# Optimization experiments

Measured on AMD Instinct MI355X. Metric: run time of the kernel, lower is better.

## Reference

```python
import jax, jax.numpy as jnp
import numpy as np

BATCH = 8192
NUM_FEATURES = 2048
NUM_CLASSES = 10
NUM_LAYERS = 2
LOGIT_SCALE = 5.0
INV_SQRT2 = 1.0 / np.sqrt(2.0)


def setup_inputs() -> dict:
    key = jax.random.key(0)
    k1, k2 = jax.random.split(key)
    # input feature phases in [-pi, pi), one oscillator thread per feature
    x = jax.random.uniform(k1, (BATCH, NUM_FEATURES), jnp.float32, -np.pi, np.pi)
    # trainable phase shifts: (num_stacks * num_layers * num_features,) ~ U(-pi, pi)
    weights = jax.random.uniform(k2, (NUM_LAYERS * NUM_FEATURES,), jnp.float32, -np.pi, np.pi)
    return {"x": x, "weights": weights}


def _vpc_forward(x, weights):
    # x: (B, N) phases; state z_i = e^{i x_i} with unit amplitude
    B, N = x.shape
    w = weights.reshape(NUM_LAYERS, N)  # per-layer shift parameters
    z = jnp.exp(1j * x)  # complex64 state vector, shape (B, N)
    for layer in range(NUM_LAYERS):
        # shift: rotate every thread phase by its trainable weight
        z = z * jnp.exp(1j * w[layer])  # broadcast (N,) over batch
        # mix: Hadamard-like 2x2 unitary on adjacent pairs (0,1),(2,3),...
        a = z[:, 0::2]
        b = z[:, 1::2]
        z = jnp.stack(((a + b) * INV_SQRT2, (a - b) * INV_SQRT2), axis=-1).reshape(B, N)
        # dft: global unitary DFT across the N threads
        z = jnp.fft.fft(z, norm="ortho")
    phases = jnp.arctan2(jnp.imag(z), jnp.real(z))  # (B, N)
    # multi-class readout: sin-smoothed phases of first K threads -> softmax
    logits = jnp.sin(phases[:, :NUM_CLASSES]) * LOGIT_SCALE
    return jax.nn.softmax(logits, axis=-1)  # (B, K)


def reference(x, weights):
    return _vpc_forward(x, weights)
```

## Files before the change

kernel.cpp:

```cpp
#include <hip/hip_runtime.h>
#include <math.h>

#define NF       2048
#define NC       10
#define THREADS  256

typedef float f2 __attribute__((ext_vector_type(2)));
typedef float f4 __attribute__((ext_vector_type(4)));

__device__ __forceinline__ f2 mk2(float a, float b){ f2 r; r.x=a; r.y=b; return r; }

__device__ __forceinline__ int swz(int i) { return i ^ (((i >> 4) & 7) << 1); }

__device__ __forceinline__ f2 cmul(f2 a, f2 b){
    f2 t = mk2(a.x, a.x) * b;
    return mk2(a.y, a.y) * mk2(-b.y, b.x) + t;
}
__device__ __forceinline__ f2 mul_mi(f2 d){ return mk2(d.y, -d.x); }
__device__ __forceinline__ f2 mul_w1(f2 d){
    const float C = 0.70710678118654752f;
    return (d + mk2(d.y, -d.x)) * mk2(C, C);
}
__device__ __forceinline__ f2 mul_w3(f2 d){
    const float C = 0.70710678118654752f;
    return (mk2(d.y, -d.y) - mk2(d.x, d.x)) * mk2(C, C);
}

template<int S>
__device__ __forceinline__ void stage8_ip(f2* __restrict__ buf,
                                          const f2* __restrict__ twl,
                                          int tid, int rbase)
{
    __syncthreads();
    f2 a0 = buf[rbase       ];
    f2 a1 = buf[rbase +  256];
    f2 a2 = buf[rbase +  512];
    f2 a3 = buf[rbase +  768];
    f2 a4 = buf[rbase + 1024];
    f2 a5 = buf[rbase + 1280];
    f2 a6 = buf[rbase + 1536];
    f2 a7 = buf[rbase + 1792];
    const int q  = tid & (S - 1);
    const int pb = tid ^ q;
    f2 w1 = twl[pb];
    __syncthreads();
    f2 u0 = a0+a4, u1 = a0-a4;
    f2 u2 = a1+a5, u3 = mul_w1(a1-a5);
    f2 u4 = a2+a6, u5 = mul_mi(a2-a6);
    f2 u6 = a3+a7, u7 = mul_w3(a3-a7);
    f2 v0 = u0+u4, v2 = u0-u4;
    f2 v1 = u1+u5, v3 = u1-u5;
    f2 v4 = u2+u6, v6 = mul_mi(u2-u6);
    f2 v5 = u3+u7, v7 = mul_mi(u3-u7);
    const int base = q + 8 * pb;
    buf[swz(base)] = v0+v4;
    f2 y4 = v0-v4;
    f2 w2 = cmul(w1,w1);
    f2 w4 = cmul(w2,w2);
    buf[swz(base + 4*S)] = cmul(y4,w4);
    f2 y1 = v1+v5, y5 = v1-v5;
    buf[swz(base +   S)] = cmul(y1,w1);
    f2 w5 = cmul(w4,w1);
    buf[swz(base + 5*S)] = cmul(y5,w5);
    f2 y2 = v2+v6, y6 = v2-v6;
    buf[swz(base + 2*S)] = cmul(y2,w2);
    f2 w6 = cmul(w4,w2);
    buf[swz(base + 6*S)] = cmul(y6,w6);
    f2 y3 = v3+v7, y7 = v3-v7;
    f2 w3 = cmul(w2,w1);
    buf[swz(base + 3*S)] = cmul(y3,w3);
    f2 w7 = cmul(w4,w3);
    buf[swz(base + 7*S)] = cmul(y7,w7);
}

__device__ __forceinline__ void stage8_trunc(f2* __restrict__ buf,
                                             const f2* __restrict__ twl,
                                             int tid, int rbase)
{
    __syncthreads();
    f2 a0 = buf[rbase       ];
    f2 a1 = buf[rbase +  256];
    f2 a2 = buf[rbase +  512];
    f2 a3 = buf[rbase +  768];
    f2 a4 = buf[rbase + 1024];
    f2 a5 = buf[rbase + 1280];
    f2 a6 = buf[rbase + 1536];
    f2 a7 = buf[rbase + 1792];
    const int q  = tid & 7;
    const int pb = tid ^ q;
    f2 w1 = twl[pb];
    __syncthreads();
    const int base = q + 8 * pb;
    buf[swz(base)] = ((a0+a4) + (a2+a6)) + ((a1+a5) + (a3+a7));
    if (q < 2) {
        f2 u1 = a0-a4;
        f2 u3 = mul_w1(a1-a5);
        f2 u5 = mul_mi(a2-a6);
        f2 u7 = mul_w3(a3-a7);
        buf[swz(base + 8)] = cmul((u1+u5) + (u3+u7), w1);
    }
}

__device__ __forceinline__ void stage4_rot_ip(f2* __restrict__ buf,
                                              const f2* __restrict__ w1r,
                                              int tid, int r2base)
{
    __syncthreads();
    f4 R0 = *(const f4*)&buf[r2base       ];
    f4 R1 = *(const f4*)&buf[r2base +  512];
    f4 R2 = *(const f4*)&buf[r2base + 1024];
    f4 R3 = *(const f4*)&buf[r2base + 1536];
    f2 u0 = R0.lo, v0 = R0.hi;
    f2 u1 = R1.lo, v1 = R1.hi;
    f2 u2 = R2.lo, v2 = R2.hi;
    f2 u3 = R3.lo, v3 = R3.hi;
    f2 us0 = u0+u2, us1 = u1+u3;
    f2 ud0 = u0-u2, ud1 = mul_mi(u1-u3);
    f2 vs0 = v0+v2, vs1 = v1+v3;
    f2 vd0 = v0-v2, vd1 = mul_mi(v1-v3);
    f2 uy[4] = { us0+us1, ud0+ud1, us0-us1, ud0-ud1 };
    f2 vy[4] = { vs0+vs1, vd0+vd1, vs0-vs1, vd0-vd1 };
    #pragma unroll
    for (int k = 0; k < 4; ++k) {
        f2 wv = w1r[tid + 256*k];
        float s0, c0, s1, c1;
        __sincosf(wv.x, &s0, &c0);
        __sincosf(wv.y, &s1, &c1);
        f2 z0 = cmul(uy[k], mk2(c0,s0));
        f2 z1 = cmul(vy[k], mk2(c1,s1));
        f4 o; o.lo = z0+z1; o.hi = z0-z1;
        *(f4*)&buf[r2base + 512*k] = o;
    }
}

__global__ __launch_bounds__(THREADS, 8) void vpc_kernel(
        const float* __restrict__ x, const float* __restrict__ w,
        float* __restrict__ out) {
    __shared__ __align__(16) f2 A[NF];
    __shared__ __align__(16) f2 twl[256];
    __shared__ float smax[NC];
    const int tid    = threadIdx.x;
    const int row    = blockIdx.x;
    const int rbase  = swz(tid);
    const int r2base = swz(2*tid);

    {
        float a = -(float)tid * (float)(M_PI / 1024.0);
        float s, c;
        __sincosf(a, &s, &c);
        twl[tid] = mk2(c, s);
    }

    const f4* xr4 = (const f4*)(x + (size_t)row * NF);
    const f4* wr4 = (const f4*)w;
    #pragma unroll
    for (int i = 0; i < 2; ++i) {
        const int g = tid + 256*i;
        f4 xv = xr4[g];
        f4 wv = wr4[g];
        float s0,c0,s1,c1,s2,c2,s3,c3;
        __sincosf(xv.x + wv.x, &s0, &c0);
        __sincosf(xv.y + wv.y, &s1, &c1);
        __sincosf(xv.z + wv.z, &s2, &c2);
        __sincosf(xv.w + wv.w, &s3, &c3);
        f2 z0 = mk2(c0,s0), z1 = mk2(c1,s1);
        f2 z2 = mk2(c2,s2), z3 = mk2(c3,s3);
        f4 o0; o0.lo = z0+z1; o0.hi = z0-z1;
        f4 o1; o1.lo = z2+z3; o1.hi = z2-z3;
        *(f4*)&A[swz(4*g)]     = o0;
        *(f4*)&A[swz(4*g + 2)] = o1;
    }

    stage8_ip<1> (A, twl, tid, rbase);
    stage8_ip<8> (A, twl, tid, rbase);
    stage8_ip<64>(A, twl, tid, rbase);
    stage4_rot_ip(A, (const f2*)(w + NF), tid, r2base);

    stage8_ip<1>(A, twl, tid, rbase);
    stage8_trunc(A, twl, tid, rbase);

    __syncthreads();
    if (tid < NC) {
        f2 acc = mk2(0.f, 0.f);
        #pragma unroll 8
        for (int r = 0; r < 32; ++r) {
            int addr = (tid + 64*r) ^ ((r & 1) << 3);
            acc = acc + A[addr];
        }
        float mag = sqrtf(acc.x*acc.x + acc.y*acc.y);
        smax[tid] = 5.0f * acc.y / fmaxf(mag, 1e-30f);
    }
    __syncthreads();
    if (tid < NC) {
        float l = smax[tid];
        float mx = smax[0];
        #pragma unroll
        for (int j = 1; j < NC; ++j) mx = fmaxf(mx, smax[j]);
        float s = 0.f;
        #pragma unroll
        for (int j = 0; j < NC; ++j) s += __expf(smax[j] - mx);
        out[(size_t)row * NC + tid] = __expf(l - mx) / s;
    }
}

extern "C" void kernel_launch(void* const* d_in, const int* in_sizes, int n_in,
                              void* d_out, int out_size, void* d_ws, size_t ws_size,
                              hipStream_t stream) {
    const float* x = (const float*)d_in[0];
    const float* w = (const float*)d_in[1];
    float* out = (float*)d_out;
    (void)d_ws; (void)ws_size;

    vpc_kernel<<<8192, THREADS, 0, stream>>>(x, w, out);
}
```

Measured before the change: 118.0 us.

## Restructure FFT into radix-4 block step plus wave-local radix-8 stages

Reorganizes the 2048-point FFT so that after one block-wide radix-4 step, each 64-lane wave performs its three radix-8 stages on a private 512-element slice without block barriers. The second FFT's truncated last stage is replaced by wave shuffle reductions that compute only the needed output bins directly. This is meant to cut the number of __syncthreads and the serial 32-element accumulation done by ten threads. In exchange it adds extra twiddle tables, shuffles and more complex swizzled indexing.

```diff
diff --git a/kernel.cpp b/kernel.cpp
--- a/kernel.cpp
+++ b/kernel.cpp
@@ -9,9 +9,6 @@
 typedef float f4 __attribute__((ext_vector_type(4)));
 
 __device__ __forceinline__ f2 mk2(float a, float b){ f2 r; r.x=a; r.y=b; return r; }
-
-__device__ __forceinline__ int swz(int i) { return i ^ (((i >> 4) & 7) << 1); }
-
 __device__ __forceinline__ f2 cmul(f2 a, f2 b){
     f2 t = mk2(a.x, a.x) * b;
     return mk2(a.y, a.y) * mk2(-b.y, b.x) + t;
@@ -26,129 +23,117 @@
     return (mk2(d.y, -d.y) - mk2(d.x, d.x)) * mk2(C, C);
 }
 
-template<int S>
-__device__ __forceinline__ void stage8_ip(f2* __restrict__ buf,
-                                          const f2* __restrict__ twl,
-                                          int tid, int rbase)
+__device__ __forceinline__ int swz(int i){ return i ^ (((i >> 4) & 7) << 1); }
+
+__device__ __forceinline__ f2 wred(f2 v){
+    #pragma unroll
+    for (int m = 32; m >= 1; m >>= 1) {
+        f2 o;
+        o.x = __shfl_xor(v.x, m, 64);
+        o.y = __shfl_xor(v.y, m, 64);
+        v = v + o;
+    }
+    return v;
+}
+
+__device__ __forceinline__ void stepA(f2* __restrict__ A_,
+                                      const f2* __restrict__ twl,
+                                      int tid, int fb)
 {
     __syncthreads();
-    f2 a0 = buf[rbase       ];
-    f2 a1 = buf[rbase +  256];
-    f2 a2 = buf[rbase +  512];
-    f2 a3 = buf[rbase +  768];
-    f2 a4 = buf[rbase + 1024];
-    f2 a5 = buf[rbase + 1280];
-    f2 a6 = buf[rbase + 1536];
-    f2 a7 = buf[rbase + 1792];
-    const int q  = tid & (S - 1);
-    const int pb = tid ^ q;
-    f2 w1 = twl[pb];
-    __syncthreads();
-    f2 u0 = a0+a4, u1 = a0-a4;
-    f2 u2 = a1+a5, u3 = mul_w1(a1-a5);
-    f2 u4 = a2+a6, u5 = mul_mi(a2-a6);
-    f2 u6 = a3+a7, u7 = mul_w3(a3-a7);
-    f2 v0 = u0+u4, v2 = u0-u4;
-    f2 v1 = u1+u5, v3 = u1-u5;
-    f2 v4 = u2+u6, v6 = mul_mi(u2-u6);
-    f2 v5 = u3+u7, v7 = mul_mi(u3-u7);
-    const int base = q + 8 * pb;
-    buf[swz(base)] = v0+v4;
-    f2 y4 = v0-v4;
-    f2 w2 = cmul(w1,w1);
-    f2 w4 = cmul(w2,w2);
-    buf[swz(base + 4*S)] = cmul(y4,w4);
-    f2 y1 = v1+v5, y5 = v1-v5;
-    buf[swz(base +   S)] = cmul(y1,w1);
-    f2 w5 = cmul(w4,w1);
-    buf[swz(base + 5*S)] = cmul(y5,w5);
-    f2 y2 = v2+v6, y6 = v2-v6;
-    buf[swz(base + 2*S)] = cmul(y2,w2);
-    f2 w6 = cmul(w4,w2);
-    buf[swz(base + 6*S)] = cmul(y6,w6);
-    f2 y3 = v3+v7, y7 = v3-v7;
-    f2 w3 = cmul(w2,w1);
-    buf[swz(base + 3*S)] = cmul(y3,w3);
-    f2 w7 = cmul(w4,w3);
-    buf[swz(base + 7*S)] = cmul(y7,w7);
-}
-
-__device__ __forceinline__ void stage8_trunc(f2* __restrict__ buf,
-                                             const f2* __restrict__ twl,
-                                             int tid, int rbase)
+    f2 a0 = A_[fb      ], a1 = A_[fb +  512], a2 = A_[fb + 1024], a3 = A_[fb + 1536];
+    f2 b0 = A_[fb + 256], b1 = A_[fb +  768], b2 = A_[fb + 1280], b3 = A_[fb + 1792];
+    f2 wa = twl[tid], wb = twl[tid + 256];
+    {
+        f2 s0 = a0+a2, s1 = a1+a3, d0 = a0-a2, d1 = mul_mi(a1-a3);
+        f2 w2 = cmul(wa,wa), w3 = cmul(w2,wa);
+        A_[fb       ] = s0 + s1;
+        A_[fb +  512] = cmul(d0 + d1, wa);
+        A_[fb + 1024] = cmul(s0 - s1, w2);
+        A_[fb + 1536] = cmul(d0 - d1, w3);
+    }
+    {
+        f2 s0 = b0+b2, s1 = b1+b3, d0 = b0-b2, d1 = mul_mi(b1-b3);
+        f2 w2 = cmul(wb,wb), w3 = cmul(w2,wb);
+        A_[fb +  256] = s0 + s1;
+        A_[fb +  768] = cmul(d0 + d1, wb);
+        A_[fb + 1280] = cmul(s0 - s1, w2);
+        A_[fb + 1792] = cmul(d0 - d1, w3);
+    }
+}
+
+template<int STAGE>
+__device__ __forceinline__ void wlstage(f2* __restrict__ A_,
+                                        const f2* __restrict__ twl,
+                                        const f2* __restrict__ tw4,
+                                        int ln, int RB, int rb0, int rb1)
 {
-    __syncthreads();
-    f2 a0 = buf[rbase       ];
-    f2 a1 = buf[rbase +  256];
-    f2 a2 = buf[rbase +  512];
-    f2 a3 = buf[rbase +  768];
-    f2 a4 = buf[rbase + 1024];
-    f2 a5 = buf[rbase + 1280];
-    f2 a6 = buf[rbase + 1536];
-    f2 a7 = buf[rbase + 1792];
-    const int q  = tid & 7;
-    const int pb = tid ^ q;
-    f2 w1 = twl[pb];
-    __syncthreads();
-    const int base = q + 8 * pb;
-    buf[swz(base)] = ((a0+a4) + (a2+a6)) + ((a1+a5) + (a3+a7));
-    if (q < 2) {
-        f2 u1 = a0-a4;
-        f2 u3 = mul_w1(a1-a5);
-        f2 u5 = mul_mi(a2-a6);
-        f2 u7 = mul_w3(a3-a7);
-        buf[swz(base + 8)] = cmul((u1+u5) + (u3+u7), w1);
-    }
-}
-
-__device__ __forceinline__ void stage4_rot_ip(f2* __restrict__ buf,
-                                              const f2* __restrict__ w1r,
-                                              int tid, int r2base)
-{
-    __syncthreads();
-    f4 R0 = *(const f4*)&buf[r2base       ];
-    f4 R1 = *(const f4*)&buf[r2base +  512];
-    f4 R2 = *(const f4*)&buf[r2base + 1024];
-    f4 R3 = *(const f4*)&buf[r2base + 1536];
-    f2 u0 = R0.lo, v0 = R0.hi;
-    f2 u1 = R1.lo, v1 = R1.hi;
-    f2 u2 = R2.lo, v2 = R2.hi;
-    f2 u3 = R3.lo, v3 = R3.hi;
-    f2 us0 = u0+u2, us1 = u1+u3;
-    f2 ud0 = u0-u2, ud1 = mul_mi(u1-u3);
-    f2 vs0 = v0+v2, vs1 = v1+v3;
-    f2 vd0 = v0-v2, vd1 = mul_mi(v1-v3);
-    f2 uy[4] = { us0+us1, ud0+ud1, us0-us1, ud0-ud1 };
-    f2 vy[4] = { vs0+vs1, vd0+vd1, vs0-vs1, vd0-vd1 };
-    #pragma unroll
-    for (int k = 0; k < 4; ++k) {
-        f2 wv = w1r[tid + 256*k];
-        float s0, c0, s1, c1;
-        __sincosf(wv.x, &s0, &c0);
-        __sincosf(wv.y, &s1, &c1);
-        f2 z0 = cmul(uy[k], mk2(c0,s0));
-        f2 z1 = cmul(vy[k], mk2(c1,s1));
-        f4 o; o.lo = z0+z1; o.hi = z0-z1;
-        *(f4*)&buf[r2base + 512*k] = o;
+    f2 a0 = A_[rb0      ], a1 = A_[rb1 +  64];
+    f2 a2 = A_[rb0 + 128], a3 = A_[rb1 + 192];
+    f2 a4 = A_[rb0 + 256], a5 = A_[rb1 + 320];
+    f2 a6 = A_[rb0 + 384], a7 = A_[rb1 + 448];
+    f2 u0 = a0+a4, u1 = a0-a4, u2 = a1+a5, u3 = mul_w1(a1-a5);
+    f2 u4 = a2+a6, u5 = mul_mi(a2-a6), u6 = a3+a7, u7 = mul_w3(a3-a7);
+    f2 v0 = u0+u4, v2 = u0-u4, v1 = u1+u5, v3 = u1-u5;
+    f2 v4 = u2+u6, v6 = mul_mi(u2-u6), v5 = u3+u7, v7 = mul_mi(u3-u7);
+    f2 y0 = v0+v4, y4 = v0-v4, y1 = v1+v5, y5 = v1-v5;
+    f2 y2 = v2+v6, y6 = v2-v6, y3 = v3+v7, y7 = v3-v7;
+    if constexpr (STAGE != 3) {
+        f2 w1 = (STAGE == 1) ? tw4[ln] : twl[32*(ln>>3)];
+        f2 w2 = cmul(w1,w1), w3 = cmul(w2,w1), w4 = cmul(w2,w2);
+        f2 w5 = cmul(w4,w1), w6 = cmul(w4,w2), w7 = cmul(w4,w3);
+        y1 = cmul(y1,w1); y2 = cmul(y2,w2); y3 = cmul(y3,w3); y4 = cmul(y4,w4);
+        y5 = cmul(y5,w5); y6 = cmul(y6,w6); y7 = cmul(y7,w7);
+    }
+    if constexpr (STAGE == 1) {
+        const int wb = RB + ((8*ln) ^ (((ln>>1)&7)<<1));
+        f4 o;
+        o.lo = y0; o.hi = y1; *(f4*)&A_[wb    ] = o;
+        o.lo = y2; o.hi = y3; *(f4*)&A_[wb ^ 2] = o;
+        o.lo = y4; o.hi = y5; *(f4*)&A_[wb ^ 4] = o;
+        o.lo = y6; o.hi = y7; *(f4*)&A_[wb ^ 6] = o;
+    } else if constexpr (STAGE == 2) {
+        const int bi = (ln & 7) + 64*(ln >> 3);
+        #define ST2(K, Y) { int wi = bi + 8*(K); wi ^= ((wi>>4)&7)<<1; A_[RB + wi] = Y; }
+        ST2(0,y0) ST2(1,y1) ST2(2,y2) ST2(3,y3)
+        ST2(4,y4) ST2(5,y5) ST2(6,y6) ST2(7,y7)
+        #undef ST2
+    } else {
+        A_[rb0      ] = y0;  A_[rb1 +  64] = y1;
+        A_[rb0 + 128] = y2;  A_[rb1 + 192] = y3;
+        A_[rb0 + 256] = y4;  A_[rb1 + 320] = y5;
+        A_[rb0 + 384] = y6;  A_[rb1 + 448] = y7;
     }
 }
 
 __global__ __launch_bounds__(THREADS, 8) void vpc_kernel(
         const float* __restrict__ x, const float* __restrict__ w,
-        float* __restrict__ out) {
+        float* __restrict__ out)
+{
     __shared__ __align__(16) f2 A[NF];
-    __shared__ __align__(16) f2 twl[256];
+    __shared__ __align__(16) f2 twl[512];
+    __shared__ __align__(16) f2 tw4[64];
     __shared__ float smax[NC];
-    const int tid    = threadIdx.x;
-    const int row    = blockIdx.x;
-    const int rbase  = swz(tid);
-    const int r2base = swz(2*tid);
-
-    {
-        float a = -(float)tid * (float)(M_PI / 1024.0);
+    const int tid = threadIdx.x;
+    const int ln  = tid & 63;
+    const int wvi = tid >> 6;
+    const int row = blockIdx.x;
+    const int RB  = wvi << 9;
+    const int sl  = ln ^ (((ln>>4)&3)<<1);
+    const int rb0 = RB + sl;
+    const int rb1 = RB + (sl ^ 8);
+    const int fb  = swz(tid);
+
+    {
         float s, c;
-        __sincosf(a, &s, &c);
+        __sincosf(-(float)tid * (float)(M_PI/1024.0), &s, &c);
         twl[tid] = mk2(c, s);
+        __sincosf(-(float)(tid + 256) * (float)(M_PI/1024.0), &s, &c);
+        twl[tid + 256] = mk2(c, s);
+        if (tid < 64) {
+            __sincosf(-(float)(4*tid) * (float)(M_PI/1024.0), &s, &c);
+            tw4[tid] = mk2(c, s);
+        }
     }
 
     const f4* xr4 = (const f4*)(x + (size_t)row * NF);
@@ -156,43 +141,77 @@
     #pragma unroll
     for (int i = 0; i < 2; ++i) {
         const int g = tid + 256*i;
-        f4 xv = xr4[g];
-        f4 wv = wr4[g];
+        f4 xv  = xr4[g];
+        f4 wv4 = wr4[g];
         float s0,c0,s1,c1,s2,c2,s3,c3;
-        __sincosf(xv.x + wv.x, &s0, &c0);
-        __sincosf(xv.y + wv.y, &s1, &c1);
-        __sincosf(xv.z + wv.z, &s2, &c2);
-        __sincosf(xv.w + wv.w, &s3, &c3);
-        f2 z0 = mk2(c0,s0), z1 = mk2(c1,s1);
-        f2 z2 = mk2(c2,s2), z3 = mk2(c3,s3);
+        __sincosf(xv.x + wv4.x, &s0, &c0);
+        __sincosf(xv.y + wv4.y, &s1, &c1);
+        __sincosf(xv.z + wv4.z, &s2, &c2);
+        __sincosf(xv.w + wv4.w, &s3, &c3);
+        f2 z0 = mk2(c0,s0), z1 = mk2(c1,s1), z2 = mk2(c2,s2), z3 = mk2(c3,s3);
         f4 o0; o0.lo = z0+z1; o0.hi = z0-z1;
         f4 o1; o1.lo = z2+z3; o1.hi = z2-z3;
         *(f4*)&A[swz(4*g)]     = o0;
         *(f4*)&A[swz(4*g + 2)] = o1;
     }
 
-    stage8_ip<1> (A, twl, tid, rbase);
-    stage8_ip<8> (A, twl, tid, rbase);
-    stage8_ip<64>(A, twl, tid, rbase);
-    stage4_rot_ip(A, (const f2*)(w + NF), tid, r2base);
-
-    stage8_ip<1>(A, twl, tid, rbase);
-    stage8_trunc(A, twl, tid, rbase);
-
+    stepA(A, twl, tid, fb);
+    __syncthreads();
+    wlstage<1>(A, twl, tw4, ln, RB, rb0, rb1);
+    __builtin_amdgcn_sched_barrier(0);
+    wlstage<2>(A, twl, tw4, ln, RB, rb0, rb1);
+    __builtin_amdgcn_sched_barrier(0);
+    wlstage<3>(A, twl, tw4, ln, RB, rb0, rb1);
+
+    __syncthreads();
+    const int pb0 = ((tid & 1) << 10) + swz(tid >> 1);
+    f2 pa0 = A[pb0      ], qa0 = A[pb0 + 512];
+    f2 pa1 = A[pb0 + 128], qa1 = A[pb0 + 640];
+    f2 pa2 = A[pb0 + 256], qa2 = A[pb0 + 768];
+    f2 pa3 = A[pb0 + 384], qa3 = A[pb0 + 896];
+    __syncthreads();
+    {
+        const f2* w1r = (const f2*)(w + NF);
+        const int wb2 = swz(2*tid);
+        #define ROT(I, PA, QA) { \
+            f2 wv2 = w1r[tid + 256*(I)]; \
+            float ss0, cc0, ss1, cc1; \
+            __sincosf(wv2.x, &ss0, &cc0); \
+            __sincosf(wv2.y, &ss1, &cc1); \
+            f2 za = cmul(PA, mk2(cc0, ss0)); \
+            f2 zb = cmul(QA, mk2(cc1, ss1)); \
+            f4 o; o.lo = za + zb; o.hi = za - zb; \
+            *(f4*)&A[wb2 + 512*(I)] = o; }
+        ROT(0, pa0, qa0) ROT(1, pa1, qa1) ROT(2, pa2, qa2) ROT(3, pa3, qa3)
+        #undef ROT
+    }
+
+    stepA(A, twl, tid, fb);
+    __syncthreads();
+    {
+        f2 a0 = A[rb0      ], a1 = A[rb1 +  64];
+        f2 a2 = A[rb0 + 128], a3 = A[rb1 + 192];
+        f2 a4 = A[rb0 + 256], a5 = A[rb1 + 320];
+        f2 a6 = A[rb0 + 384], a7 = A[rb1 + 448];
+        f2 e04 = a0+a4, e26 = a2+a6, e15 = a1+a5, e37 = a3+a7;
+        f2 y0 = (e04 + e26) + (e15 + e37);
+        f2 u1 = a0-a4, u3 = mul_w1(a1-a5), u5 = mul_mi(a2-a6), u7 = mul_w3(a3-a7);
+        f2 W  = tw4[ln];
+        f2 y1 = cmul((u1+u5) + (u3+u7), W);
+        f2 y2 = cmul((e04 - e26) + mul_mi(e15 - e37), cmul(W, W));
+        y0 = wred(y0); y1 = wred(y1); y2 = wred(y2);
+        if (ln < 3) {
+            f2 X = (ln == 0) ? y0 : ((ln == 1) ? y1 : y2);
+            int bin = wvi + 4*ln;
+            if (bin < NC) {
+                float mag = sqrtf(X.x*X.x + X.y*X.y);
+                smax[bin] = 5.0f * X.y / fmaxf(mag, 1e-30f);
+            }
+        }
+    }
     __syncthreads();
     if (tid < NC) {
-        f2 acc = mk2(0.f, 0.f);
-        #pragma unroll 8
-        for (int r = 0; r < 32; ++r) {
-            int addr = (tid + 64*r) ^ ((r & 1) << 3);
-            acc = acc + A[addr];
-        }
-        float mag = sqrtf(acc.x*acc.x + acc.y*acc.y);
-        smax[tid] = 5.0f * acc.y / fmaxf(mag, 1e-30f);
-    }
-    __syncthreads();
-    if (tid < NC) {
-        float l = smax[tid];
+        float l  = smax[tid];
         float mx = smax[0];
         #pragma unroll
         for (int j = 1; j < NC; ++j) mx = fmaxf(mx, smax[j]);
```

Result: slower. 137.6 us (+16.6%).
